# Optimization experiments

Hardware: AMD Instinct MI355X
Metric: run time of the kernel (lower is better)

## Reference

```python
import jax, jax.numpy as jnp
import numpy as np

N_POINTS = 262144
NUM_LEVELS = 16
LEVEL_DIM = 8
BASE_RES = 16
LOG2_HASH = 21
BOUNDS = 10.0
TEXT_REP = 512
IMAGE_REP = 512
MLP_WIDTH = 256
PRIMES = (1, 2654435761, 805459861)  # instant-NGP fast_hash primes


def _level_layout():
    # mirrors torch-ngp GridEncoder offset computation
    max_params = 2 ** LOG2_HASH
    sizes, offsets = [], [0]
    for l in range(NUM_LEVELS):
        res = int(np.ceil(BASE_RES * (2.0 ** l)))
        p = min(max_params, res ** 3)
        p = int(np.ceil(p / 8) * 8)  # align to 8
        sizes.append(p)
        offsets.append(offsets[-1] + p)
    return sizes, offsets

SIZES, OFFSETS = _level_layout()
TOTAL_PARAMS = OFFSETS[-1]  # ~27.56M rows


def grid_encode(u, embeddings):
    """u: [N,3] in [0,1]; torch-ngp kernel remaps with bound=1: u=(u+1)/2.
    With this config (res+1)^3 > hashmap_size at every level, so the hash
    path is always taken (faithful to get_grid_index)."""
    u = (u + 1.0) * 0.5
    feats = []
    for l in range(NUM_LEVELS):
        scale = 2.0 ** l * BASE_RES - 1.0          # exp2(l*log2(s))*H - 1
        pos = u * scale + 0.5                       # align_corners=False
        base = jnp.floor(pos)
        frac = pos - base                           # [N,3] trilinear fracs
        pg = base.astype(jnp.uint32)
        acc = jnp.zeros((u.shape[0], LEVEL_DIM), dtype=u.dtype)
        for corner in range(8):
            bits = [(corner >> d) & 1 for d in range(3)]
            cpos = pg + jnp.asarray(bits, dtype=jnp.uint32)
            w = jnp.prod(jnp.where(jnp.asarray(bits, dtype=bool), frac, 1.0 - frac), axis=-1)
            h = (cpos[:, 0] * jnp.uint32(PRIMES[0])
                 ^ cpos[:, 1] * jnp.uint32(PRIMES[1])
                 ^ cpos[:, 2] * jnp.uint32(PRIMES[2]))  # uint32 wraparound hash
            idx = (h % jnp.uint32(SIZES[l])).astype(jnp.int32) + OFFSETS[l]
            acc = acc + w[:, None] * embeddings[idx]    # gather [N,8]
        feats.append(acc)
    return jnp.concatenate(feats, axis=-1)              # [N, 128]


def setup_inputs() -> dict:
    key = jax.random.key(0)
    ks = jax.random.split(key, 8)
    x = jax.random.uniform(ks[0], (N_POINTS, 3), jnp.float32, -BOUNDS, BOUNDS)
    emb = jax.random.uniform(ks[1], (TOTAL_PARAMS, LEVEL_DIM), jnp.float32, -1e-4, 1e-4)
    d_in = NUM_LEVELS * LEVEL_DIM  # 128
    d_out = TEXT_REP + IMAGE_REP   # 1024
    W1 = jax.random.normal(ks[2], (d_in, MLP_WIDTH), jnp.float32) * (1.0 / np.sqrt(d_in))
    b1 = jnp.zeros((MLP_WIDTH,), jnp.float32)
    W2 = jax.random.normal(ks[3], (MLP_WIDTH, MLP_WIDTH), jnp.float32) * (1.0 / np.sqrt(MLP_WIDTH))
    b2 = jnp.zeros((MLP_WIDTH,), jnp.float32)
    W3 = jax.random.normal(ks[4], (MLP_WIDTH, d_out), jnp.float32) * (1.0 / np.sqrt(MLP_WIDTH))
    b3 = jnp.zeros((d_out,), jnp.float32)
    return {"x": x, "embeddings": emb, "W1": W1, "b1": b1, "W2": W2, "b2": b2, "W3": W3, "b3": b3}


def reference(x, embeddings, W1, b1, W2, b2, W3, b3):
    # bound normalization: (x - min) / (max - min), min=-10, max=+10
    bounded = (x + BOUNDS) / (2.0 * BOUNDS)
    gh = grid_encode(bounded, embeddings)
    h = jax.nn.relu(gh @ W1 + b1)
    h = jax.nn.relu(h @ W2 + b2)
    out = h @ W3 + b3
    label_latent = out[..., :TEXT_REP]
    image_latent = out[..., TEXT_REP:TEXT_REP + IMAGE_REP]  # image head = Identity
    return (label_latent, image_latent)
```

## Files before the change

### kernel.cpp

```cpp
#include <hip/hip_runtime.h>
#include <cstdint>

#pragma STDC FP_CONTRACT OFF


typedef _Float16 f16;
typedef __attribute__((ext_vector_type(8))) _Float16 f16x8;
typedef __attribute__((ext_vector_type(4))) float f32x4;

#define ACT_SCALE 4096.0f
#define INV_ACT_SCALE (1.0f / 4096.0f)

__device__ __forceinline__ void gld16(const void* g, void* l) {
  __builtin_amdgcn_global_load_lds(
      (const __attribute__((address_space(1))) void*)(uintptr_t)g,
      (__attribute__((address_space(3))) void*)(uint32_t)(uintptr_t)l,
      16, 0, 0);
}

__global__ __launch_bounds__(256) void grid_encode_kernel(
    const float* __restrict__ x, const float* __restrict__ emb,
    f16* __restrict__ gh, int p0, int npts)
{
#pragma clang fp contract(off)
  int g = blockIdx.x * blockDim.x + threadIdx.x;
  if (g >= npts * 16) return;
  int pl = g >> 4;
  int l  = g & 15;
  int p  = p0 + pl;

  float x0 = x[3 * p + 0];
  float x1 = x[3 * p + 1];
  float x2 = x[3 * p + 2];

  float t0 = (x0 + 10.0f) * 0.05f;
  float t1 = (x1 + 10.0f) * 0.05f;
  float t2 = (x2 + 10.0f) * 0.05f;
  asm volatile("" : "+v"(t0), "+v"(t1), "+v"(t2));
  float u0 = (t0 + 1.0f) * 0.5f;
  float u1 = (t1 + 1.0f) * 0.5f;
  float u2 = (t2 + 1.0f) * 0.5f;
  asm volatile("" : "+v"(u0), "+v"(u1), "+v"(u2));

  float scale = (float)((16 << l) - 1);
  float pos0 = u0 * scale + 0.5f;
  float pos1 = u1 * scale + 0.5f;
  float pos2 = u2 * scale + 0.5f;

  float fb0 = floorf(pos0), fb1 = floorf(pos1), fb2 = floorf(pos2);
  float f0 = pos0 - fb0;
  float f1 = pos1 - fb1;
  float f2 = pos2 - fb2;
  uint32_t px = (uint32_t)fb0, py = (uint32_t)fb1, pz = (uint32_t)fb2;

  uint32_t mask = (l < 3) ? ((4096u << (3 * l)) - 1u) : 2097151u;
  uint32_t off;
  if (l == 0)      off = 0u;
  else if (l == 1) off = 4096u;
  else if (l == 2) off = 36864u;
  else             off = 299008u + (uint32_t)(l - 3) * 2097152u;

  float wx[2] = {1.0f - f0, f0};
  float wy[2] = {1.0f - f1, f1};
  float wz[2] = {1.0f - f2, f2};

  float acc[8];
#pragma unroll
  for (int j = 0; j < 8; ++j) acc[j] = 0.0f;

#pragma unroll
  for (int c = 0; c < 8; ++c) {
    uint32_t cx = px + (uint32_t)(c & 1);
    uint32_t cy = py + (uint32_t)((c >> 1) & 1);
    uint32_t cz = pz + (uint32_t)((c >> 2) & 1);
    float w = wx[c & 1] * wy[(c >> 1) & 1] * wz[(c >> 2) & 1];
    uint32_t h = cx ^ (cy * 2654435761u) ^ (cz * 805459861u);
    uint32_t idx = (h & mask) + off;
    const float4* e = (const float4*)(emb + (size_t)idx * 8);
    float4 e0 = e[0];
    float4 e1 = e[1];
    float m0 = w * e0.x, m1 = w * e0.y, m2 = w * e0.z, m3 = w * e0.w;
    float m4 = w * e1.x, m5 = w * e1.y, m6 = w * e1.z, m7 = w * e1.w;
    asm volatile("" : "+v"(m0), "+v"(m1), "+v"(m2), "+v"(m3),
                      "+v"(m4), "+v"(m5), "+v"(m6), "+v"(m7));
    acc[0] += m0; acc[1] += m1; acc[2] += m2; acc[3] += m3;
    acc[4] += m4; acc[5] += m5; acc[6] += m6; acc[7] += m7;
  }

  f16x8 o;
#pragma unroll
  for (int j = 0; j < 8; ++j) o[j] = (f16)(acc[j] * ACT_SCALE);
  *(f16x8*)&gh[(size_t)pl * 128 + l * 8] = o;
}

template <int K, int N>
__global__ __launch_bounds__(256) void prep_w(
    const float* __restrict__ W, f16* __restrict__ Wt)
{
  int i = blockIdx.x * 256 + threadIdx.x;
  if (i >= N * K) return;
  int n = i / K, k = i - n * K;
  Wt[i] = (f16)W[(size_t)k * N + n];
}

__global__ __launch_bounds__(256) void prep_w1f(
    const float* __restrict__ W1, f16* __restrict__ Wf1)
{
  int i = blockIdx.x * 256 + threadIdx.x;
  if (i >= 128 * 256) return;
  int e  = i & 7;
  int lr = (i >> 3) & 15;
  int kg = (i >> 7) & 15;
  int q  = i >> 11;
  int n = q * 16 + lr;
  int k = kg * 8 + e;
  Wf1[i] = (f16)W1[(size_t)k * 256 + n];
}

__global__ __launch_bounds__(256) void prep_w2f(
    const float* __restrict__ W2, f16* __restrict__ Wf2)
{
  int i = blockIdx.x * 256 + threadIdx.x;
  if (i >= 256 * 256) return;
  int e  = i & 7;
  int lr = (i >> 3) & 15;
  int kg = (i >> 7) & 31;
  int q  = i >> 12;
  int n = q * 16 + lr;
  int k = kg * 8 + e;
  Wf2[i] = (f16)W2[(size_t)k * 256 + n];
}

__global__ __launch_bounds__(512) void fused_mlp(
    const f16* __restrict__ gh, const f16* __restrict__ Wf1,
    const float* __restrict__ b1, const f16* __restrict__ Wf2,
    const float* __restrict__ b2, const f16* __restrict__ Wt3,
    const float* __restrict__ b3, float* __restrict__ out,
    int rowBase, int nTotal)
{
  __shared__ alignas(16) f16 H1[128 * 256];
  __shared__ alignas(16) f16 H2[128 * 256];
  __shared__ float B3s[1024];

  const int tid  = threadIdx.x;
  const int lane = tid & 63;
  const int wid  = tid >> 6;
  const int bm   = blockIdx.x * 128;
  const int lr   = lane & 15;
  const int lkg  = lane >> 4;

  auto stage3 = [&](int buf, int c) {
#pragma unroll
    for (int s = 0; s < 2; ++s) {
      const int g   = tid + s * 512;
      const int row = g >> 5;
      const int sg  = g & 31;
      const int gs  = (sg & 24) | ((sg ^ row) & 7);
      gld16(&Wt3[(size_t)(c * 32 + row) * 256 + gs * 8],
            &H1[buf * 8192 + g * 8]);
    }
  };

#pragma unroll
  for (int s = 0; s < 4; ++s) {
    const int g   = tid + s * 512;
    const int row = g >> 4;
    const int sg  = g & 15;
    const int gs  = (sg & 8) | ((sg ^ row) & 7);
    gld16(&gh[(size_t)(bm + row) * 128 + gs * 8], &H2[g * 8]);
  }
  B3s[tid] = b3[tid];
  B3s[tid + 512] = b3[tid + 512];
  __syncthreads();

  {
    const int rowg = wid >> 2, colg = wid & 3;
    f16x8 bf1[4][4];
#pragma unroll
    for (int j = 0; j < 4; ++j)
#pragma unroll
      for (int f = 0; f < 4; ++f)
        bf1[j][f] = *(const f16x8*)&Wf1[(((colg * 4 + j) * 16 + f * 4 + lkg) * 16 + lr) * 8];

    f32x4 acc[4][4];
#pragma unroll
    for (int i = 0; i < 4; ++i)
#pragma unroll
      for (int j = 0; j < 4; ++j) acc[i][j] = (f32x4){0.f, 0.f, 0.f, 0.f};

#pragma unroll
    for (int f = 0; f < 4; ++f) {
      f16x8 af[4];
#pragma unroll
      for (int i = 0; i < 4; ++i) {
        const int r  = rowg * 64 + i * 16 + lr;
        const int kg = f * 4 + lkg;
        const int gs = (kg & 8) | ((kg ^ r) & 7);
        af[i] = *(const f16x8*)&H2[r * 128 + gs * 8];
      }
#pragma unroll
      for (int i = 0; i < 4; ++i)
#pragma unroll
        for (int j = 0; j < 4; ++j)
          acc[i][j] = __builtin_amdgcn_mfma_f32_16x16x32_f16(
              af[i], bf1[j][f], acc[i][j], 0, 0, 0);
    }

#pragma unroll
    for (int i = 0; i < 4; ++i)
#pragma unroll
      for (int j = 0; j < 4; ++j) {
        const int col = colg * 64 + j * 16 + lr;
        const float bv = b1[col];
        const int kg = col >> 3, e = col & 7;
#pragma unroll
        for (int q = 0; q < 4; ++q) {
          const int row = rowg * 64 + i * 16 + lkg * 4 + q;
          const int kgs = (kg & 24) | ((kg ^ row) & 7);
          float v = fmaxf(acc[i][j][q] + bv * ACT_SCALE, 0.0f);
          H1[row * 256 + kgs * 8 + e] = (f16)v;
        }
      }
  }
  __syncthreads();

  {
    const int rowg = wid >> 2, colg = wid & 3;
    f16x8 bf2[4][8];
#pragma unroll
    for (int j = 0; j < 4; ++j)
#pragma unroll
      for (int f = 0; f < 8; ++f)
        bf2[j][f] = *(const f16x8*)&Wf2[(((colg * 4 + j) * 32 + f * 4 + lkg) * 16 + lr) * 8];

    f32x4 acc[4][4];
#pragma unroll
    for (int i = 0; i < 4; ++i)
#pragma unroll
      for (int j = 0; j < 4; ++j) acc[i][j] = (f32x4){0.f, 0.f, 0.f, 0.f};

#pragma unroll
    for (int f = 0; f < 8; ++f) {
      f16x8 af[4];
#pragma unroll
      for (int i = 0; i < 4; ++i) {
        const int r   = rowg * 64 + i * 16 + lr;
        const int kg  = f * 4 + lkg;
        const int kgs = (kg & 24) | ((kg ^ r) & 7);
        af[i] = *(const f16x8*)&H1[r * 256 + kgs * 8];
      }
#pragma unroll
      for (int i = 0; i < 4; ++i)
#pragma unroll
        for (int j = 0; j < 4; ++j)
          acc[i][j] = __builtin_amdgcn_mfma_f32_16x16x32_f16(
              af[i], bf2[j][f], acc[i][j], 0, 0, 0);
    }

#pragma unroll
    for (int i = 0; i < 4; ++i)
#pragma unroll
      for (int j = 0; j < 4; ++j) {
        const int col = colg * 64 + j * 16 + lr;
        const float bv = b2[col];
        const int kg = col >> 3, e = col & 7;
#pragma unroll
        for (int q = 0; q < 4; ++q) {
          const int row = rowg * 64 + i * 16 + lkg * 4 + q;
          const int kgs = (kg & 24) | ((kg ^ row) & 7);
          float v = fmaxf(acc[i][j][q] + bv * ACT_SCALE, 0.0f);
          H2[row * 256 + kgs * 8 + e] = (f16)v;
        }
      }
  }
  __syncthreads();

  f16x8 af3[8];
#pragma unroll
  for (int f = 0; f < 8; ++f) {
    const int r   = wid * 16 + lr;
    const int kg  = f * 4 + lkg;
    const int kgs = (kg & 24) | ((kg ^ r) & 7);
    af3[f] = *(const f16x8*)&H2[r * 256 + kgs * 8];
  }

  stage3(0, 0);
  stage3(1, 1);
  stage3(2, 2);
  __syncthreads();

  auto body3 = [&](int c, int wmode, bool dostage) {
    if (wmode == 18) {
      asm volatile("s_waitcnt vmcnt(18)" ::: "memory");
      __builtin_amdgcn_sched_barrier(0);
    } else if (wmode == 16) {
      asm volatile("s_waitcnt vmcnt(16)" ::: "memory");
      __builtin_amdgcn_sched_barrier(0);
    }
    const int buf = c % 3;
    f16x8 bf3[2][8];
#pragma unroll
    for (int cg = 0; cg < 2; ++cg)
#pragma unroll
      for (int f = 0; f < 8; ++f) {
        const int n   = cg * 16 + lr;
        const int kg  = f * 4 + lkg;
        const int kgs = (kg & 24) | ((kg ^ n) & 7);
        bf3[cg][f] = *(const f16x8*)&H1[buf * 8192 + (n * 32 + kgs) * 8];
      }
    asm volatile("s_waitcnt lgkmcnt(0)" ::: "memory");
    __builtin_amdgcn_sched_barrier(0);
    __builtin_amdgcn_s_barrier();
    __builtin_amdgcn_sched_barrier(0);
    if (dostage) stage3(buf, c + 3);
    f32x4 a[2];
#pragma unroll
    for (int cg = 0; cg < 2; ++cg) {
      a[cg] = (f32x4){0.f, 0.f, 0.f, 0.f};
#pragma unroll
      for (int f = 0; f < 8; ++f)
        a[cg] = __builtin_amdgcn_mfma_f32_16x16x32_f16(af3[f], bf3[cg][f],
                                                       a[cg], 0, 0, 0);
    }
#pragma unroll
    for (int cg = 0; cg < 2; ++cg) {
      const int col = c * 32 + cg * 16 + lr;
      const float bv = B3s[col];
#pragma unroll
      for (int q = 0; q < 4; ++q) {
        const int row = bm + wid * 16 + lkg * 4 + q;
        float v = a[cg][q] * INV_ACT_SCALE + bv;
        size_t grow = (size_t)(rowBase + row);
        float* dst = (col < 512)
                         ? (out + grow * 512 + col)
                         : (out + (size_t)nTotal * 512 + grow * 512 + (col - 512));
        __builtin_nontemporal_store(v, dst);
      }
    }
  };

  body3(0, 18, true);
  body3(1, 18, true);
  for (int c = 2; c <= 28; ++c) body3(c, 18, true);
  body3(29, 18, false);
  body3(30, 16, false);
  body3(31, 16, false);
}

extern "C" void kernel_launch(void* const* d_in, const int* in_sizes, int n_in,
                              void* d_out, int out_size, void* d_ws, size_t ws_size,
                              hipStream_t stream)
{
  const float* x   = (const float*)d_in[0];
  const float* emb = (const float*)d_in[1];
  const float* W1  = (const float*)d_in[2];
  const float* b1  = (const float*)d_in[3];
  const float* W2  = (const float*)d_in[4];
  const float* b2  = (const float*)d_in[5];
  const float* W3  = (const float*)d_in[6];
  const float* b3  = (const float*)d_in[7];
  float* out = (float*)d_out;

  const int NPTS = in_sizes[0] / 3;

  f16* Wf1 = (f16*)d_ws;
  f16* Wf2 = Wf1 + 128 * 256;
  f16* Wt3 = Wf2 + 256 * 256;
  f16* gh0 = Wt3 + 256 * 1024;
  const size_t wtBytes = (size_t)(128 * 256 + 256 * 256 + 256 * 1024) * sizeof(f16);

  long long cmax = (long long)((ws_size - wtBytes) / 256);
  int C = (int)((cmax / 128) * 128);
  if (C > NPTS) C = NPTS;
  if (C < 128) C = 128;

  prep_w1f<<<(128 * 256 + 255) / 256, 256, 0, stream>>>(W1, Wf1);
  prep_w2f<<<(256 * 256 + 255) / 256, 256, 0, stream>>>(W2, Wf2);
  prep_w<256, 1024><<<(256 * 1024 + 255) / 256, 256, 0, stream>>>(W3, Wt3);

  for (int p0 = 0; p0 < NPTS; p0 += C) {
    int cur = (NPTS - p0 < C) ? (NPTS - p0) : C;

    int nthr = cur * 16;
    grid_encode_kernel<<<(nthr + 255) / 256, 256, 0, stream>>>(x, emb, gh0, p0, cur);

    fused_mlp<<<cur / 128, 512, 0, stream>>>(gh0, Wf1, b1, Wf2, b2, Wt3, b3,
                                             out, p0, NPTS);
  }
}
```

Before: 767.6 us.

## Encode hash grid level-by-level in groups with level-major feature layout

The grid encoder now runs as several launches, each covering a small group of levels for all points, with threads mapped point-fastest within a level. Features are stored level-major instead of point-major. The intent is to keep each level's hash table slice resident in cache while all points gather from it, cutting random DRAM traffic on the embedding table. The chunked loop over points is removed, so the whole point set is encoded before a single MLP launch. This assumes the workspace can hold the full feature buffer, and the MLP's feature loads become strided across level planes.

```diff
diff --git a/kernel.cpp b/kernel.cpp
--- a/kernel.cpp
+++ b/kernel.cpp
@@ -20,14 +20,13 @@
 
 __global__ __launch_bounds__(256) void grid_encode_kernel(
     const float* __restrict__ x, const float* __restrict__ emb,
-    f16* __restrict__ gh, int p0, int npts)
+    f16* __restrict__ gh, int l0, int nlev, int npts)
 {
 #pragma clang fp contract(off)
   int g = blockIdx.x * blockDim.x + threadIdx.x;
-  if (g >= npts * 16) return;
-  int pl = g >> 4;
-  int l  = g & 15;
-  int p  = p0 + pl;
+  if (g >= npts * nlev) return;
+  int p = g % npts;
+  int l = l0 + g / npts;
 
   float x0 = x[3 * p + 0];
   float x1 = x[3 * p + 1];
@@ -90,7 +89,7 @@
   f16x8 o;
 #pragma unroll
   for (int j = 0; j < 8; ++j) o[j] = (f16)(acc[j] * ACT_SCALE);
-  *(f16x8*)&gh[(size_t)pl * 128 + l * 8] = o;
+  *(f16x8*)&gh[((size_t)l * npts + p) * 8] = o;
 }
 
 template <int K, int N>
@@ -136,7 +135,7 @@
     const float* __restrict__ b1, const f16* __restrict__ Wf2,
     const float* __restrict__ b2, const f16* __restrict__ Wt3,
     const float* __restrict__ b3, float* __restrict__ out,
-    int rowBase, int nTotal)
+    int nTotal)
 {
   __shared__ alignas(16) f16 H1[128 * 256];
   __shared__ alignas(16) f16 H2[128 * 256];
@@ -167,7 +166,7 @@
     const int row = g >> 4;
     const int sg  = g & 15;
     const int gs  = (sg & 8) | ((sg ^ row) & 7);
-    gld16(&gh[(size_t)(bm + row) * 128 + gs * 8], &H2[g * 8]);
+    gld16(&gh[((size_t)gs * nTotal + (bm + row)) * 8], &H2[g * 8]);
   }
   B3s[tid] = b3[tid];
   B3s[tid + 512] = b3[tid + 512];
@@ -330,7 +329,7 @@
       for (int q = 0; q < 4; ++q) {
         const int row = bm + wid * 16 + lkg * 4 + q;
         float v = a[cg][q] * INV_ACT_SCALE + bv;
-        size_t grow = (size_t)(rowBase + row);
+        size_t grow = (size_t)row;
         float* dst = (col < 512)
                          ? (out + grow * 512 + col)
                          : (out + (size_t)nTotal * 512 + grow * 512 + (col - 512));
@@ -367,24 +366,20 @@
   f16* Wf2 = Wf1 + 128 * 256;
   f16* Wt3 = Wf2 + 256 * 256;
   f16* gh0 = Wt3 + 256 * 1024;
-  const size_t wtBytes = (size_t)(128 * 256 + 256 * 256 + 256 * 1024) * sizeof(f16);
-
-  long long cmax = (long long)((ws_size - wtBytes) / 256);
-  int C = (int)((cmax / 128) * 128);
-  if (C > NPTS) C = NPTS;
-  if (C < 128) C = 128;
 
   prep_w1f<<<(128 * 256 + 255) / 256, 256, 0, stream>>>(W1, Wf1);
   prep_w2f<<<(256 * 256 + 255) / 256, 256, 0, stream>>>(W2, Wf2);
   prep_w<256, 1024><<<(256 * 1024 + 255) / 256, 256, 0, stream>>>(W3, Wt3);
 
-  for (int p0 = 0; p0 < NPTS; p0 += C) {
-    int cur = (NPTS - p0 < C) ? (NPTS - p0) : C;
-
-    int nthr = cur * 16;
-    grid_encode_kernel<<<(nthr + 255) / 256, 256, 0, stream>>>(x, emb, gh0, p0, cur);
-
-    fused_mlp<<<cur / 128, 512, 0, stream>>>(gh0, Wf1, b1, Wf2, b2, Wt3, b3,
-                                             out, p0, NPTS);
-  }
-}
+  const int groups[8][2] = {{0, 3}, {3, 2}, {5, 2}, {7, 2},
+                            {9, 2}, {11, 2}, {13, 2}, {15, 1}};
+  for (int gi = 0; gi < 8; ++gi) {
+    const int l0 = groups[gi][0], nl = groups[gi][1];
+    const int nthr = NPTS * nl;
+    grid_encode_kernel<<<(nthr + 255) / 256, 256, 0, stream>>>(
+        x, emb, gh0, l0, nl, NPTS);
+  }
+
+  fused_mlp<<<NPTS / 128, 512, 0, stream>>>(gh0, Wf1, b1, Wf2, b2, Wt3, b3,
+                                            out, NPTS);
+}
```

Result: faster. 744.3 us (-3.0%).
